# Kernel optimization log

Measured on AMD Instinct MI355X. Metric: run time of the kernel, lower is better.

Reference implementation:

```python
import jax, jax.numpy as jnp
import numpy as np

B = 2048; H = 300; L = 128; N = 131072


def _gru_dir(x, h0, w_ih, w_hh, b_ih, b_hh, reverse):
    # x: [B, L, H]; torch GRU gate order: r, z, n
    xp = jnp.einsum('blh,gh->blg', x, w_ih) + b_ih      # [B, L, 3H]
    xp = jnp.moveaxis(xp, 1, 0)                          # [L, B, 3H]

    def step(h, xp_t):
        xr, xz, xn = jnp.split(xp_t, 3, axis=-1)
        hp = h @ w_hh.T + b_hh
        hr, hz, hn = jnp.split(hp, 3, axis=-1)
        r = jax.nn.sigmoid(xr + hr)
        z = jax.nn.sigmoid(xz + hz)
        n = jnp.tanh(xn + r * hn)
        h_new = (1.0 - z) * n + z * h
        return h_new, h_new

    _, ys = jax.lax.scan(step, h0, xp, reverse=reverse)
    return jnp.moveaxis(ys, 0, 1)                        # [B, L, H]


def setup_inputs() -> dict:
    key = jax.random.key(0)
    ks = jax.random.split(key, 12)
    # ragged segment lengths: sum == N, max == L, min >= 1
    rng = np.random.default_rng(0)
    lengths = np.full(B, 64, dtype=np.int32)
    lengths[0] = 128; lengths[1] = 32; lengths[2] = 32
    d = rng.integers(0, 64, size=1022)
    lengths[4::2] = 64 + d
    lengths[5::2] = 64 - d
    assert lengths.sum() == N and lengths.max() == L and lengths.min() >= 1
    s = 1.0 / np.sqrt(H)
    u = lambda k, shape: jax.random.uniform(k, shape, jnp.float32, -s, s)
    return {
        'node': jax.random.normal(ks[0], (N, H), jnp.float32),
        'a_scope': jnp.asarray(lengths, jnp.int32),
        'max_len': L,
        'bias': u(ks[1], (H,)),
        'w_ih_f': u(ks[2], (3 * H, H)),
        'w_hh_f': u(ks[3], (3 * H, H)),
        'b_ih_f': u(ks[4], (3 * H,)),
        'b_hh_f': u(ks[5], (3 * H,)),
        'w_ih_b': u(ks[6], (3 * H, H)),
        'w_hh_b': u(ks[7], (3 * H, H)),
        'b_ih_b': u(ks[8], (3 * H,)),
        'b_hh_b': u(ks[9], (3 * H,)),
    }


def reference(node, a_scope, max_len, bias, w_ih_f, w_hh_f, b_ih_f, b_hh_f,
              w_ih_b, w_hh_b, b_ih_b, b_hh_b):
    n_total = node.shape[0]
    message = jax.nn.relu(node + bias)
    ends = jnp.cumsum(a_scope)
    starts = ends - a_scope
    pos = jnp.arange(max_len)
    idx = jnp.clip(starts[:, None] + pos[None, :], 0, n_total - 1)   # [B, L]
    valid = pos[None, :] < a_scope[:, None]                          # [B, L]
    # initial hidden: per-segment max of raw node features
    gathered = node[idx]                                             # [B, L, H]
    h0 = jnp.max(jnp.where(valid[..., None], gathered, -jnp.inf), axis=1)  # [B, H]
    # zero-padded messages (padding rows ARE processed by the GRU, as in torch)
    msg_pad = jnp.where(valid[..., None], message[idx], 0.0)         # [B, L, H]
    out_f = _gru_dir(msg_pad, h0, w_ih_f, w_hh_f, b_ih_f, b_hh_f, reverse=False)
    out_b = _gru_dir(msg_pad, h0, w_ih_b, w_hh_b, b_ih_b, b_hh_b, reverse=True)
    out = jnp.concatenate([out_f, out_b], axis=-1)                   # [B, L, 2H]
    # unpad back to flat ragged layout [N, 2H]
    n_idx = jnp.arange(n_total)
    b_idx = jnp.searchsorted(ends, n_idx, side='right')
    l_idx = n_idx - starts[b_idx]
    return out[b_idx, l_idx]
```

## Files before the change

kernel.cpp:

```cpp
#include <hip/hip_runtime.h>
#include <cstddef>
#include <cstdint>


typedef short s8v __attribute__((ext_vector_type(8)));
typedef float f4v __attribute__((ext_vector_type(4)));

#define NSEG   2048
#define HID    300
#define HPAD   320
#define MAXLEN 128
#define NTOT   131072
#define PKSTRIDE 307200

__device__ __forceinline__ short f2bf(float f){
  unsigned u = __float_as_uint(f);
  u = (u + 0x7FFFu + ((u >> 16) & 1u)) >> 16;
  return (short)u;
}
__device__ __forceinline__ float bf2f(unsigned short u){
  return __uint_as_float((unsigned)u << 16);
}
__device__ __forceinline__ float sigm(float x){ return 1.f / (1.f + __expf(-x)); }
__device__ __forceinline__ float tanha(float x){ return 1.f - 2.f / (__expf(2.f * x) + 1.f); }

__global__ __launch_bounds__(1024)
void scan_starts_k(const int* __restrict__ a_scope, int* __restrict__ starts){
  __shared__ int buf[2][NSEG];
  const int tid = threadIdx.x;
  for (int i = tid; i < NSEG; i += 1024) buf[0][i] = a_scope[i];
  __syncthreads();
  int src = 0;
  for (int off = 1; off < NSEG; off <<= 1){
    for (int i = tid; i < NSEG; i += 1024){
      int v = buf[src][i];
      if (i >= off) v += buf[src][i - off];
      buf[1 - src][i] = v;
    }
    __syncthreads();
    src ^= 1;
  }
  for (int i = tid; i < NSEG; i += 1024) starts[i] = buf[src][i] - a_scope[i];
}

__global__ void h0_max_k(const float* __restrict__ node, const int* __restrict__ a_scope,
                         const int* __restrict__ starts, float* __restrict__ h0){
  const int b = blockIdx.x;
  const int k = threadIdx.x;
  const int s = starts[b], len = a_scope[b];
  float m = 0.f;
  if (k < HID){
    m = -3.402823466e38f;
    const float* p = node + (size_t)s * HID + k;
    for (int t = 0; t < len; ++t) m = fmaxf(m, p[(size_t)t * HID]);
  }
  h0[(size_t)b * HPAD + k] = m;
}

__global__ void prep2_k(const float* __restrict__ wih_f, const float* __restrict__ whh_f,
                        const float* __restrict__ bih_f, const float* __restrict__ bhh_f,
                        const float* __restrict__ wih_b, const float* __restrict__ whh_b,
                        const float* __restrict__ bih_b, const float* __restrict__ bhh_b,
                        short* __restrict__ PkH, short* __restrict__ PkI,
                        float* __restrict__ gbias){
  const int idx = blockIdx.x * 256 + threadIdx.x;
  if (idx < 1228800){
    const bool isH = idx < 614400;
    int t = isH ? idx : idx - 614400;
    int e = t & 7, lane = (t >> 3) & 63;
    int r = t >> 9;
    int kt = r % 10; r /= 10;
    int jt = r % 20; r /= 20;
    int sec = r % 3, d = r / 3;
    const float* w = isH ? (d ? whh_b : whh_f) : (d ? wih_b : wih_f);
    int j = jt * 16 + (lane & 15);
    int k = kt * 32 + (lane >> 4) * 8 + e;
    float v = 0.f;
    if (j < HID && k < HID) v = w[(sec * HID + j) * HID + k];
    (isH ? PkH : PkI)[t] = f2bf(v);
  } else if (idx < 1228800 + 2560){
    int r3 = idx - 1228800;
    int d = r3 / 1280;
    int rem = r3 - d * 1280;
    int sec = rem / HPAD;
    int j = rem - sec * HPAD;
    const float* bih = d ? bih_b : bih_f;
    const float* bhh = d ? bhh_b : bhh_f;
    float v = 0.f;
    if (j < HID){
      if (sec == 0)      v = bih[j] + bhh[j];
      else if (sec == 1) v = bih[HID + j] + bhh[HID + j];
      else if (sec == 2) v = bih[2 * HID + j];
      else               v = bhh[2 * HID + j];
    }
    gbias[r3] = v;
  }
}

__global__ __launch_bounds__(256)
void xp_gemm_k(const float* __restrict__ node, const float* __restrict__ bias,
               const short* __restrict__ PkI, short* __restrict__ xp){
  __shared__ __align__(16) short Bt[4 * 5120];
  const int dir = blockIdx.x & 1;
  const int blk = blockIdx.x >> 1;
  const int tid = threadIdx.x;
  const int wave = tid >> 6, lane = tid & 63;
  const int quad = lane >> 4, lc = lane & 15, l8 = lane << 3;
  const int rowbase = blk * 128 + wave * 32;
  const short* PI = PkI + (size_t)dir * PKSTRIDE;
  short* xpd = xp + (size_t)dir * ((size_t)NTOT * 900);

  s8v A[2][10];
  #pragma unroll
  for (int tm = 0; tm < 2; ++tm){
    const float* src = node + (size_t)(rowbase + tm * 16 + lc) * HID;
    #pragma unroll
    for (int kt = 0; kt < 10; ++kt){
      const int k0 = kt * 32 + quad * 8;
      s8v a;
      #pragma unroll
      for (int e = 0; e < 8; ++e){
        const int k = k0 + e;
        float v = 0.f;
        if (k < HID){ v = src[k] + bias[k]; v = v > 0.f ? v : 0.f; }
        a[e] = f2bf(v);
      }
      A[tm][kt] = a;
    }
  }

  for (int st0 = 0; st0 < 60; st0 += 4){
    __syncthreads();
    for (int i = tid; i < 2560; i += 256)
      ((s8v*)Bt)[i] = ((const s8v*)(PI + (size_t)st0 * 5120))[i];
    __syncthreads();
    #pragma unroll
    for (int u = 0; u < 4; ++u){
      const int st = st0 + u;
      const int sec = st / 20, jt = st % 20;
      f4v a0 = {0.f,0.f,0.f,0.f}, a1 = {0.f,0.f,0.f,0.f};
      #pragma unroll
      for (int kt = 0; kt < 10; ++kt){
        const s8v b = *(const s8v*)&Bt[u * 5120 + kt * 512 + l8];
        a0 = __builtin_amdgcn_mfma_f32_16x16x32_bf16(A[0][kt], b, a0, 0, 0, 0);
        a1 = __builtin_amdgcn_mfma_f32_16x16x32_bf16(A[1][kt], b, a1, 0, 0, 0);
      }
      const int j = jt * 16 + lc;
      if (j < HID){
        const int g = sec * HID + j;
        #pragma unroll
        for (int r = 0; r < 4; ++r){
          const int rr = rowbase + quad * 4 + r;
          xpd[(size_t)rr * 900 + g]        = f2bf(a0[r]);
          xpd[(size_t)(rr + 16) * 900 + g] = f2bf(a1[r]);
        }
      }
    }
  }
}

__global__ __launch_bounds__(640)
void gru3_k(const int* __restrict__ a_scope, const int* __restrict__ starts,
            const float* __restrict__ h0, const short* __restrict__ PkH,
            const float* __restrict__ gbias, const short* __restrict__ xp,
            float* __restrict__ out){
  __shared__ __align__(16) short hbuf[16][328];

  const int dir  = blockIdx.x & 1;
  const int seg0 = (blockIdx.x >> 1) * 16;
  const int tid  = threadIdx.x;
  const int wave = tid >> 6;
  const int lane = tid & 63;
  const int quad = lane >> 4;
  const int lc   = lane & 15;
  const int l8   = lane << 3;
  const int jt0  = 2 * wave;

  int ls_r[4], ll_r[4];
  #pragma unroll
  for (int r = 0; r < 4; ++r){
    const int m = quad * 4 + r;
    ls_r[r] = starts[seg0 + m];
    ll_r[r] = a_scope[seg0 + m];
  }

  for (int i = tid; i < 16 * HPAD; i += 640){
    const int m = i / HPAD, k = i - m * HPAD;
    hbuf[m][k] = f2bf(h0[(size_t)(seg0 + m) * HPAD + k]);
  }

  float hprev[2][4];
  float bR[2], bZ[2], bX[2], bH[2];
  bool  jv[2];
  #pragma unroll
  for (int i = 0; i < 2; ++i){
    const int jt = jt0 + i;
    const int j  = jt * 16 + lc;
    jv[i] = (jt < 19) && (j < HID);
    bR[i] = bZ[i] = bX[i] = bH[i] = 0.f;
    hprev[i][0] = hprev[i][1] = hprev[i][2] = hprev[i][3] = 0.f;
    if (jv[i]){
      bR[i] = gbias[dir * 1280 + 0 * HPAD + j];
      bZ[i] = gbias[dir * 1280 + 1 * HPAD + j];
      bX[i] = gbias[dir * 1280 + 2 * HPAD + j];
      bH[i] = gbias[dir * 1280 + 3 * HPAD + j];
      #pragma unroll
      for (int r = 0; r < 4; ++r)
        hprev[i][r] = h0[(size_t)(seg0 + quad * 4 + r) * HPAD + j];
    }
  }
  __syncthreads();

  const short* PH = PkH + (size_t)dir * PKSTRIDE;
  const unsigned short* xpd = (const unsigned short*)xp + (size_t)dir * ((size_t)NTOT * 900);
  const int njt = (jt0 < 18) ? 2 : 1;

  for (int step = 0; step < MAXLEN; ++step){
    const int t = dir ? (MAXLEN - 1 - step) : step;

    float xg[2][4][3];
    #pragma unroll
    for (int i = 0; i < 2; ++i){
      const int j = (jt0 + i) * 16 + lc;
      #pragma unroll
      for (int r = 0; r < 4; ++r){
        float vr = 0.f, vz = 0.f, vn = 0.f;
        if (jv[i] && t < ll_r[r]){
          const unsigned short* p = xpd + (size_t)(ls_r[r] + t) * 900 + j;
          vr = bf2f(p[0]); vz = bf2f(p[300]); vn = bf2f(p[600]);
        }
        xg[i][r][0] = vr; xg[i][r][1] = vz; xg[i][r][2] = vn;
      }
    }

    __syncthreads();

    f4v acc[2][3];
    #pragma unroll
    for (int i = 0; i < 2; ++i)
      #pragma unroll
      for (int s = 0; s < 3; ++s)
        acc[i][s] = f4v{0.f, 0.f, 0.f, 0.f};

    #pragma unroll 2
    for (int kt = 0; kt < 10; ++kt){
      const s8v a = *(const s8v*)&hbuf[lc][kt * 32 + quad * 8];
      #pragma unroll
      for (int i = 0; i < 2; ++i){
        if (i < njt){
          const int jt = jt0 + i;
          #pragma unroll
          for (int s = 0; s < 3; ++s){
            const s8v b = *(const s8v*)(PH + (size_t)((s * 20 + jt) * 10 + kt) * 512 + l8);
            acc[i][s] = __builtin_amdgcn_mfma_f32_16x16x32_bf16(a, b, acc[i][s], 0, 0, 0);
          }
        }
      }
    }
    __syncthreads();

    #pragma unroll
    for (int i = 0; i < 2; ++i){
      if (jv[i]){
        const int j = (jt0 + i) * 16 + lc;
        #pragma unroll
        for (int r = 0; r < 4; ++r){
          const int m = quad * 4 + r;
          const float rg = sigm(acc[i][0][r] + bR[i] + xg[i][r][0]);
          const float zg = sigm(acc[i][1][r] + bZ[i] + xg[i][r][1]);
          const float ng = tanha(xg[i][r][2] + bX[i] + rg * (acc[i][2][r] + bH[i]));
          const float hnew = (1.f - zg) * ng + zg * hprev[i][r];
          hprev[i][r] = hnew;
          hbuf[m][j] = f2bf(hnew);
          if (t < ll_r[r])
            out[(size_t)(ls_r[r] + t) * 600 + dir * HID + j] = hnew;
        }
      }
    }
  }
}

__global__ void prep_k(const float* __restrict__ wih_f, const float* __restrict__ whh_f,
                       const float* __restrict__ bih_f, const float* __restrict__ bhh_f,
                       const float* __restrict__ wih_b, const float* __restrict__ whh_b,
                       const float* __restrict__ bih_b, const float* __restrict__ bhh_b,
                       short* __restrict__ PkA, short* __restrict__ PkB,
                       float* __restrict__ gbias){
  const int idx = blockIdx.x * 256 + threadIdx.x;
  if (idx < 819200){
    int e = idx & 7, lane = (idx >> 3) & 63;
    int r = idx >> 9;
    int kt = r % 20; r /= 20;
    int jt = r % 20; r /= 20;
    int sec = r & 1, d = r >> 1;
    const float* wih = d ? wih_b : wih_f;
    const float* whh = d ? whh_b : whh_f;
    int j = jt * 16 + (lane & 15);
    int k = kt * 32 + (lane >> 4) * 8 + e;
    float v = 0.f;
    if (j < HID){
      int row = sec * HID + j;
      if (k < HID)                    v = wih[row * HID + k];
      else if (k >= 320 && k < 620)   v = whh[row * HID + (k - 320)];
    }
    PkA[idx] = f2bf(v);
  } else if (idx < 819200 + 409600){
    int t = idx - 819200;
    int e = t & 7, lane = (t >> 3) & 63;
    int r = t >> 9;
    int kt = r % 10; r /= 10;
    int jt = r % 20; r /= 20;
    int sec = r & 1, d = r >> 1;
    const float* w = sec ? (d ? whh_b : whh_f) : (d ? wih_b : wih_f);
    int j = jt * 16 + (lane & 15);
    int k = kt * 32 + (lane >> 4) * 8 + e;
    float v = 0.f;
    if (j < HID && k < HID) v = w[(600 + j) * HID + k];
    PkB[t] = f2bf(v);
  } else if (idx < 819200 + 409600 + 2560){
    int r3 = idx - 819200 - 409600;
    int d = r3 / 1280;
    int rem = r3 - d * 1280;
    int sec = rem / HPAD;
    int j = rem - sec * HPAD;
    const float* bih = d ? bih_b : bih_f;
    const float* bhh = d ? bhh_b : bhh_f;
    float v = 0.f;
    if (j < HID){
      if (sec == 0)      v = bih[j] + bhh[j];
      else if (sec == 1) v = bih[HID + j] + bhh[HID + j];
      else if (sec == 2) v = bih[2 * HID + j];
      else               v = bhh[2 * HID + j];
    }
    gbias[r3] = v;
  }
}

__global__ __launch_bounds__(256)
void gru_k(const float* __restrict__ node, const float* __restrict__ bias,
           const int* __restrict__ a_scope, const int* __restrict__ starts,
           const float* __restrict__ h0, const short* __restrict__ PkA,
           const short* __restrict__ PkB, const float* __restrict__ gbias,
           float* __restrict__ out){
  __shared__ __align__(16) short xbuf[16][328];
  __shared__ __align__(16) short hbuf[16][328];
  __shared__ float hfp[16][324];
  __shared__ float lbias[4][HPAD];
  __shared__ int ls[16], ll[16];

  const int dir  = blockIdx.x & 1;
  const int seg0 = (blockIdx.x >> 1) * 16;
  const int tid  = threadIdx.x;
  const int wave = tid >> 6;
  const int lane = tid & 63;
  const int quad = lane >> 4;
  const int lc   = lane & 15;
  const int l8   = lane << 3;

  if (tid < 16){ ls[tid] = starts[seg0 + tid]; ll[tid] = a_scope[seg0 + tid]; }
  for (int i = tid; i < 4 * HPAD; i += 256) ((float*)lbias)[i] = gbias[dir * (4 * HPAD) + i];
  for (int i = tid; i < 16 * HPAD; i += 256){
    int m = i / HPAD, k = i - m * HPAD;
    float v = h0[(size_t)(seg0 + m) * HPAD + k];
    hfp[m][k] = v;
    hbuf[m][k] = f2bf(v);
  }
  __syncthreads();

  const short* PA = PkA + (size_t)dir * 409600;
  const short* PB = PkB + (size_t)dir * 204800;
  const int xm = tid >> 4, xu = tid & 15;

  for (int step = 0; step < MAXLEN; ++step){
    const int t = dir ? (MAXLEN - 1 - step) : step;
    {
      const bool valid = t < ll[xm];
      const float* src = node + (size_t)(ls[xm] + t) * HID;
      for (int k = xu; k < HPAD; k += 16){
        float v = 0.f;
        if (valid && k < HID){
          v = src[k] + bias[k];
          v = v > 0.f ? v : 0.f;
        }
        xbuf[xm][k] = f2bf(v);
      }
    }
    __syncthreads();

    f4v aR[5], aZ[5], aX[5], aH[5];
    #pragma unroll
    for (int i = 0; i < 5; ++i){
      aR[i] = f4v{0.f,0.f,0.f,0.f}; aZ[i] = f4v{0.f,0.f,0.f,0.f};
      aX[i] = f4v{0.f,0.f,0.f,0.f}; aH[i] = f4v{0.f,0.f,0.f,0.f};
    }
    #pragma unroll 2
    for (int kt = 0; kt < 10; ++kt){
      const int k0 = kt * 32 + quad * 8;
      const s8v a = *(const s8v*)&xbuf[lc][k0];
      #pragma unroll
      for (int i = 0; i < 5; ++i){
        const int jt = wave * 5 + i;
        const s8v bR = *(const s8v*)(PA + (size_t)((jt)      * 20 + kt) * 512 + l8);
        aR[i] = __builtin_amdgcn_mfma_f32_16x16x32_bf16(a, bR, aR[i], 0, 0, 0);
        const s8v bZ = *(const s8v*)(PA + (size_t)((20 + jt) * 20 + kt) * 512 + l8);
        aZ[i] = __builtin_amdgcn_mfma_f32_16x16x32_bf16(a, bZ, aZ[i], 0, 0, 0);
        const s8v bX = *(const s8v*)(PB + (size_t)((jt)      * 10 + kt) * 512 + l8);
        aX[i] = __builtin_amdgcn_mfma_f32_16x16x32_bf16(a, bX, aX[i], 0, 0, 0);
      }
    }
    #pragma unroll 2
    for (int kt = 0; kt < 10; ++kt){
      const int k0 = kt * 32 + quad * 8;
      const s8v a = *(const s8v*)&hbuf[lc][k0];
      #pragma unroll
      for (int i = 0; i < 5; ++i){
        const int jt = wave * 5 + i;
        const s8v bR = *(const s8v*)(PA + (size_t)((jt)      * 20 + 10 + kt) * 512 + l8);
        aR[i] = __builtin_amdgcn_mfma_f32_16x16x32_bf16(a, bR, aR[i], 0, 0, 0);
        const s8v bZ = *(const s8v*)(PA + (size_t)((20 + jt) * 20 + 10 + kt) * 512 + l8);
        aZ[i] = __builtin_amdgcn_mfma_f32_16x16x32_bf16(a, bZ, aZ[i], 0, 0, 0);
        const s8v bH = *(const s8v*)(PB + (size_t)((20 + jt) * 10 + kt) * 512 + l8);
        aH[i] = __builtin_amdgcn_mfma_f32_16x16x32_bf16(a, bH, aH[i], 0, 0, 0);
      }
    }
    __syncthreads();

    #pragma unroll
    for (int i = 0; i < 5; ++i){
      const int j = wave * 80 + i * 16 + lc;
      if (j < HID){
        const float bR = lbias[0][j], bZ = lbias[1][j];
        const float bX = lbias[2][j], bH = lbias[3][j];
        #pragma unroll
        for (int r = 0; r < 4; ++r){
          const int m = quad * 4 + r;
          const float rg = sigm(aR[i][r] + bR);
          const float zg = sigm(aZ[i][r] + bZ);
          const float ng = tanha(aX[i][r] + bX + rg * (aH[i][r] + bH));
          const float hold = hfp[m][j];
          const float hnew = (1.f - zg) * ng + zg * hold;
          hfp[m][j] = hnew;
          hbuf[m][j] = f2bf(hnew);
          if (t < ll[m])
            out[(size_t)(ls[m] + t) * 600 + dir * HID + j] = hnew;
        }
      }
    }
  }
}

extern "C" void kernel_launch(void* const* d_in, const int* in_sizes, int n_in,
                              void* d_out, int out_size, void* d_ws, size_t ws_size,
                              hipStream_t stream){
  const float* node    = (const float*)d_in[0];
  const int*   a_scope = (const int*)  d_in[1];
  const float* bias    = (const float*)d_in[3];
  const float* wih_f   = (const float*)d_in[4];
  const float* whh_f   = (const float*)d_in[5];
  const float* bih_f   = (const float*)d_in[6];
  const float* bhh_f   = (const float*)d_in[7];
  const float* wih_b   = (const float*)d_in[8];
  const float* whh_b   = (const float*)d_in[9];
  const float* bih_b   = (const float*)d_in[10];
  const float* bhh_b   = (const float*)d_in[11];
  float* out = (float*)d_out;

  char* ws = (char*)d_ws;
  int*   starts = (int*)  (ws + 0);
  float* h0     = (float*)(ws + 8192);

  scan_starts_k<<<1, 1024, 0, stream>>>(a_scope, starts);
  h0_max_k<<<NSEG, HPAD, 0, stream>>>(node, a_scope, starts, h0);

  const size_t FAST_NEED = 476956672ull;
  if (ws_size >= FAST_NEED){
    short* PkH = (short*)(ws + 2629632);
    short* PkI = (short*)(ws + 3858432);
    float* gb  = (float*)(ws + 5087232);
    short* xpb = (short*)(ws + 5097472);
    prep2_k<<<4810, 256, 0, stream>>>(wih_f, whh_f, bih_f, bhh_f,
                                      wih_b, whh_b, bih_b, bhh_b, PkH, PkI, gb);
    xp_gemm_k<<<2048, 256, 0, stream>>>(node, bias, PkI, xpb);
    gru3_k<<<256, 640, 0, stream>>>(a_scope, starts, h0, PkH, gb, xpb, out);
  } else {
    short* PkA   = (short*)(ws + 2629632);
    short* PkB   = (short*)(ws + 4268032);
    float* gbias = (float*)(ws + 5087232);
    prep_k<<<4810, 256, 0, stream>>>(wih_f, whh_f, bih_f, bhh_f,
                                     wih_b, whh_b, bih_b, bhh_b, PkA, PkB, gbias);
    gru_k<<<256, 256, 0, stream>>>(node, bias, a_scope, starts, h0, PkA, PkB, gbias, out);
  }
}
```

Baseline: 2.164 ms.

## Sort segments by length, skip padded forward steps, cache recurrent weights in registers/LDS

```diff
diff --git a/kernel.cpp b/kernel.cpp
--- a/kernel.cpp
+++ b/kernel.cpp
@@ -55,6 +55,30 @@
     for (int t = 0; t < len; ++t) m = fmaxf(m, p[(size_t)t * HID]);
   }
   h0[(size_t)b * HPAD + k] = m;
+}
+
+__global__ __launch_bounds__(256)
+void sort_segs_k(const int* __restrict__ a_scope, int* __restrict__ perm,
+                 int* __restrict__ gmax){
+  __shared__ int cnt[MAXLEN + 1];
+  __shared__ int sp[NSEG];
+  const int tid = threadIdx.x;
+  for (int i = tid; i < MAXLEN + 1; i += 256) cnt[i] = 0;
+  __syncthreads();
+  for (int i = tid; i < NSEG; i += 256) atomicAdd(&cnt[MAXLEN - a_scope[i]], 1);
+  __syncthreads();
+  if (tid == 0){
+    int s = 0;
+    for (int b = 0; b <= MAXLEN; ++b){ int c = cnt[b]; cnt[b] = s; s += c; }
+  }
+  __syncthreads();
+  for (int i = tid; i < NSEG; i += 256){
+    int p = atomicAdd(&cnt[MAXLEN - a_scope[i]], 1);
+    sp[p] = i;
+  }
+  __syncthreads();
+  for (int i = tid; i < NSEG; i += 256) perm[i] = sp[i];
+  for (int g = tid; g < NSEG / 16; g += 256) gmax[g] = a_scope[sp[g * 16]];
 }
 
 __global__ void prep2_k(const float* __restrict__ wih_f, const float* __restrict__ whh_f,
@@ -159,15 +183,18 @@
   }
 }
 
-__global__ __launch_bounds__(640)
-void gru3_k(const int* __restrict__ a_scope, const int* __restrict__ starts,
+__global__ __launch_bounds__(640, 3)
+void gru4_k(const int* __restrict__ a_scope, const int* __restrict__ starts,
+            const int* __restrict__ perm, const int* __restrict__ gmax,
             const float* __restrict__ h0, const short* __restrict__ PkH,
             const float* __restrict__ gbias, const short* __restrict__ xp,
             float* __restrict__ out){
+  __shared__ __align__(16) short WL[114 * 512];
   __shared__ __align__(16) short hbuf[16][328];
 
   const int dir  = blockIdx.x & 1;
-  const int seg0 = (blockIdx.x >> 1) * 16;
+  const int g    = blockIdx.x >> 1;
+  const int seg0 = g * 16;
   const int tid  = threadIdx.x;
   const int wave = tid >> 6;
   const int lane = tid & 63;
@@ -175,18 +202,48 @@
   const int lc   = lane & 15;
   const int l8   = lane << 3;
   const int jt0  = 2 * wave;
+  const int njt  = (jt0 < 18) ? 2 : 1;
+
+  const short* PH = PkH + (size_t)dir * PKSTRIDE;
+
+  s8v Bp[2][3][3];
+  #pragma unroll
+  for (int i = 0; i < 2; ++i){
+    #pragma unroll
+    for (int s = 0; s < 3; ++s){
+      #pragma unroll
+      for (int kt = 0; kt < 3; ++kt){
+        if (i < njt)
+          Bp[i][s][kt] = *(const s8v*)(PH + (size_t)((s * 20 + jt0 + i) * 10 + kt) * 512 + l8);
+      }
+    }
+  }
+
+  #pragma unroll
+  for (int i = 0; i < 2; ++i){
+    if (i < njt){
+      #pragma unroll
+      for (int s = 0; s < 3; ++s){
+        #pragma unroll
+        for (int ktl = 0; ktl < 2; ++ktl){
+          *(s8v*)&WL[(size_t)(wave * 12 + (i * 3 + s) * 2 + ktl) * 512 + l8] =
+            *(const s8v*)(PH + (size_t)((s * 20 + jt0 + i) * 10 + 3 + ktl) * 512 + l8);
+        }
+      }
+    }
+  }
 
   int ls_r[4], ll_r[4];
   #pragma unroll
   for (int r = 0; r < 4; ++r){
-    const int m = quad * 4 + r;
-    ls_r[r] = starts[seg0 + m];
-    ll_r[r] = a_scope[seg0 + m];
+    const int sg = perm[seg0 + quad * 4 + r];
+    ls_r[r] = starts[sg];
+    ll_r[r] = a_scope[sg];
   }
 
   for (int i = tid; i < 16 * HPAD; i += 640){
     const int m = i / HPAD, k = i - m * HPAD;
-    hbuf[m][k] = f2bf(h0[(size_t)(seg0 + m) * HPAD + k]);
+    hbuf[m][k] = f2bf(h0[(size_t)perm[seg0 + m] * HPAD + k]);
   }
 
   float hprev[2][4];
@@ -206,16 +263,15 @@
       bH[i] = gbias[dir * 1280 + 3 * HPAD + j];
       #pragma unroll
       for (int r = 0; r < 4; ++r)
-        hprev[i][r] = h0[(size_t)(seg0 + quad * 4 + r) * HPAD + j];
-    }
-  }
-  __syncthreads();
-
-  const short* PH = PkH + (size_t)dir * PKSTRIDE;
+        hprev[i][r] = h0[(size_t)perm[seg0 + quad * 4 + r] * HPAD + j];
+    }
+  }
+  __syncthreads();
+
   const unsigned short* xpd = (const unsigned short*)xp + (size_t)dir * ((size_t)NTOT * 900);
-  const int njt = (jt0 < 18) ? 2 : 1;
-
-  for (int step = 0; step < MAXLEN; ++step){
+  const int nsteps = dir ? MAXLEN : gmax[g];
+
+  for (int step = 0; step < nsteps; ++step){
     const int t = dir ? (MAXLEN - 1 - step) : step;
 
     float xg[2][4][3];
@@ -242,16 +298,41 @@
       for (int s = 0; s < 3; ++s)
         acc[i][s] = f4v{0.f, 0.f, 0.f, 0.f};
 
-    #pragma unroll 2
-    for (int kt = 0; kt < 10; ++kt){
+    #pragma unroll
+    for (int kt = 0; kt < 3; ++kt){
       const s8v a = *(const s8v*)&hbuf[lc][kt * 32 + quad * 8];
       #pragma unroll
       for (int i = 0; i < 2; ++i){
         if (i < njt){
-          const int jt = jt0 + i;
+          #pragma unroll
+          for (int s = 0; s < 3; ++s)
+            acc[i][s] = __builtin_amdgcn_mfma_f32_16x16x32_bf16(a, Bp[i][s][kt], acc[i][s], 0, 0, 0);
+        }
+      }
+    }
+    #pragma unroll
+    for (int ktl = 0; ktl < 2; ++ktl){
+      const s8v a = *(const s8v*)&hbuf[lc][(3 + ktl) * 32 + quad * 8];
+      #pragma unroll
+      for (int i = 0; i < 2; ++i){
+        if (i < njt){
           #pragma unroll
           for (int s = 0; s < 3; ++s){
-            const s8v b = *(const s8v*)(PH + (size_t)((s * 20 + jt) * 10 + kt) * 512 + l8);
+            const s8v b = *(const s8v*)&WL[(size_t)(wave * 12 + (i * 3 + s) * 2 + ktl) * 512 + l8];
+            acc[i][s] = __builtin_amdgcn_mfma_f32_16x16x32_bf16(a, b, acc[i][s], 0, 0, 0);
+          }
+        }
+      }
+    }
+    #pragma unroll 2
+    for (int kt = 5; kt < 10; ++kt){
+      const s8v a = *(const s8v*)&hbuf[lc][kt * 32 + quad * 8];
+      #pragma unroll
+      for (int i = 0; i < 2; ++i){
+        if (i < njt){
+          #pragma unroll
+          for (int s = 0; s < 3; ++s){
+            const s8v b = *(const s8v*)(PH + (size_t)((s * 20 + jt0 + i) * 10 + kt) * 512 + l8);
             acc[i][s] = __builtin_amdgcn_mfma_f32_16x16x32_bf16(a, b, acc[i][s], 0, 0, 0);
           }
         }
@@ -478,10 +559,13 @@
     short* PkI = (short*)(ws + 3858432);
     float* gb  = (float*)(ws + 5087232);
     short* xpb = (short*)(ws + 5097472);
+    int* perm = (int*)(ws + 3858432);
+    int* gmx  = (int*)(ws + 3858432 + 8192);
     prep2_k<<<4810, 256, 0, stream>>>(wih_f, whh_f, bih_f, bhh_f,
                                       wih_b, whh_b, bih_b, bhh_b, PkH, PkI, gb);
     xp_gemm_k<<<2048, 256, 0, stream>>>(node, bias, PkI, xpb);
-    gru3_k<<<256, 640, 0, stream>>>(a_scope, starts, h0, PkH, gb, xpb, out);
+    sort_segs_k<<<1, 256, 0, stream>>>(a_scope, perm, gmx);
+    gru4_k<<<256, 640, 0, stream>>>(a_scope, starts, perm, gmx, h0, PkH, gb, xpb, out);
   } else {
     short* PkA   = (short*)(ws + 2629632);
     short* PkB   = (short*)(ws + 4268032);
```

New measurement: 3.144 ms. 1.45x slower.
